# Kernel tuning notes

Hardware: AMD Instinct MI355X
Metric: run time of the kernel (lower is better)

The kernel has to match this reference:

```python
import jax, jax.numpy as jnp
import numpy as np

B, S, D, H = 1, 2048, 1024, 16
HD = D // H
THRESHOLD_PCT = 0.95
SPARSITY = 0.9
TOPK = max(1, int(S * (1.0 - SPARSITY)))  # 204


def setup_inputs() -> dict:
    key = jax.random.key(0)
    ks = jax.random.split(key, 6)
    inp = {
        'x': jax.random.normal(ks[0], (B, S, D), dtype=jnp.float32),
        'Wq': jax.random.normal(ks[1], (D, D), dtype=jnp.float32) * 0.02,
        'bq': jnp.zeros((D,), jnp.float32),
        'Wk': jax.random.normal(ks[2], (D, D), dtype=jnp.float32) * 0.02,
        'bk': jnp.zeros((D,), jnp.float32),
        'Wv': jax.random.normal(ks[3], (D, D), dtype=jnp.float32) * 0.02,
        'bv': jnp.zeros((D,), jnp.float32),
        'Wo': jax.random.normal(ks[4], (D, D), dtype=jnp.float32) * 0.02,
        'bo': jnp.zeros((D,), jnp.float32),
    }
    return inp


def _heads(t):  # [B,S,D] -> [B,H,S,HD]
    return t.reshape(B, S, H, HD).transpose(0, 2, 1, 3)


def reference(x, Wq, bq, Wk, bk, Wv, bv, Wo, bo):
    q = _heads(x @ Wq + bq)
    k = _heads(x @ Wk + bk)
    v = _heads(x @ Wv + bv)
    scores = jnp.einsum('bhqd,bhkd->bhqk', q, k) / jnp.sqrt(jnp.float32(HD))

    # --- dynamic threshold mask (per batch,head quantile over all S*S scores) ---
    flat = scores.reshape(B, H, S * S)
    thr = jnp.quantile(flat, THRESHOLD_PCT, axis=-1)[..., None, None]  # [B,H,1,1]
    thresh_mask = scores >= thr
    # fallback: if kept fraction exceeds (1 - sparsity_ratio), use per-row top-k
    cond = jnp.mean(thresh_mask.astype(scores.dtype)) > (1.0 - SPARSITY)
    kth = jax.lax.top_k(scores, TOPK)[0][..., -1:]  # k-th largest per row
    topk_mask = scores >= kth
    mask = jnp.where(cond, topk_mask, thresh_mask)

    masked = jnp.where(mask, scores, -jnp.inf)
    attn = jax.nn.softmax(masked, axis=-1)
    out = jnp.einsum('bhqk,bhkd->bhqd', attn, v)
    out = out.transpose(0, 2, 1, 3).reshape(B, S, D)
    return out @ Wo + bo
```

## Files before the change

kernel.cpp:

```cpp
#include <hip/hip_runtime.h>
#include <math.h>

#define SS 2048
#define DD 1024
#define HH 16
#define CAPC 327680u
#define LCAP 2048
#define RBIN 4

#define K_A 3984587u
#define K_B 3984588u
#define QFRAC 0.85f
#define WSCALE 2048.0f
#define WSCALE_INV (1.0f/2048.0f)
#define ESHIFT 4.0f
#define PLANE 2097152
#define NSAMP_RANK 124518u

typedef _Float16 f16x8 __attribute__((ext_vector_type(8)));
typedef _Float16 f16x4 __attribute__((ext_vector_type(4)));
typedef float    f32x4 __attribute__((ext_vector_type(4)));

__device__ __forceinline__ unsigned sortkey(float f) {
  unsigned b = __float_as_uint(f);
  return (b & 0x80000000u) ? ~b : (b | 0x80000000u);
}
__device__ __forceinline__ float inv_sortkey(unsigned u) {
  unsigned b = (u & 0x80000000u) ? (u ^ 0x80000000u) : ~u;
  return __uint_as_float(b);
}

__global__ __launch_bounds__(256) void split_x(const float* __restrict__ x,
                                               _Float16* __restrict__ xh,
                                               _Float16* __restrict__ xl)
{
  const int i = blockIdx.x * 256 + threadIdx.x;
  float4 v = ((const float4*)x)[i];
  float vv[4] = {v.x, v.y, v.z, v.w};
  f16x4 h, l;
#pragma unroll
  for (int j = 0; j < 4; ++j) {
    _Float16 hh = (_Float16)vv[j];
    h[j] = hh;
    l[j] = (_Float16)(vv[j] - (float)hh);
  }
  ((f16x4*)xh)[i] = h;
  ((f16x4*)xl)[i] = l;
}

__global__ __launch_bounds__(256) void split_wT(const float* __restrict__ Wq,
                                                const float* __restrict__ Wk,
                                                const float* __restrict__ Wv,
                                                const float* __restrict__ Wo,
                                                _Float16* __restrict__ wplanes)
{
  const int z = blockIdx.z;
  const float* W = (z == 0) ? Wq : (z == 1) ? Wk : (z == 2) ? Wv : Wo;
  _Float16* WhT = wplanes + (size_t)(2*z)     * (1024*1024);
  _Float16* WlT = wplanes + (size_t)(2*z + 1) * (1024*1024);
  __shared__ float tile[64][65];
  const int t  = threadIdx.x;
  const int r  = t >> 2;
  const int c0 = (t & 3) * 16;
  const int k0 = blockIdx.y * 64;
  const int n0 = blockIdx.x * 64;
#pragma unroll
  for (int j = 0; j < 4; ++j) {
    float4 v = *(const float4*)&W[(size_t)(k0 + r) * 1024 + n0 + c0 + j*4];
    tile[r][c0+j*4+0] = v.x; tile[r][c0+j*4+1] = v.y;
    tile[r][c0+j*4+2] = v.z; tile[r][c0+j*4+3] = v.w;
  }
  __syncthreads();
  f16x8 h0, h1, l0, l1;
#pragma unroll
  for (int j = 0; j < 8; ++j) {
    float v = tile[c0 + j][r] * WSCALE;
    _Float16 h = (_Float16)v;
    h0[j] = h; l0[j] = (_Float16)(v - (float)h);
  }
#pragma unroll
  for (int j = 0; j < 8; ++j) {
    float v = tile[c0 + 8 + j][r] * WSCALE;
    _Float16 h = (_Float16)v;
    h1[j] = h; l1[j] = (_Float16)(v - (float)h);
  }
  const size_t o = (size_t)(n0 + r) * 1024 + k0 + c0;
  *(f16x8*)&WhT[o]     = h0;
  *(f16x8*)&WhT[o + 8] = h1;
  *(f16x8*)&WlT[o]     = l0;
  *(f16x8*)&WlT[o + 8] = l1;
}

__device__ __forceinline__ void gemm_mfma_part(const _Float16* __restrict__ Ah,
                                               const _Float16* __restrict__ Al,
                                               const _Float16* __restrict__ BhT,
                                               const _Float16* __restrict__ BlT,
                                               float* __restrict__ pout,
                                               int bm, int bn, int kh)
{
  const int wave = threadIdx.x >> 6, lane = threadIdx.x & 63;
  const int wr = wave >> 1, wc = wave & 1;
  const int m0 = bm * 128 + wr * 64;
  const int n0 = bn * 128 + wc * 64;
  const int lr = lane & 15;
  const int ko = lane >> 4;

  f32x4 acc[4][4];
#pragma unroll
  for (int i = 0; i < 4; ++i)
#pragma unroll
    for (int j = 0; j < 4; ++j) acc[i][j] = (f32x4){0.f, 0.f, 0.f, 0.f};

  for (int kk = kh*16; kk < kh*16 + 16; ++kk) {
    const int kof = kk*32 + ko*8;
    f16x8 aH[4], aL[4], bH[4], bL[4];
#pragma unroll
    for (int i = 0; i < 4; ++i) {
      const size_t aoff = (size_t)(m0 + i*16 + lr) * 1024 + kof;
      aH[i] = *(const f16x8*)(Ah + aoff);
      aL[i] = *(const f16x8*)(Al + aoff);
      const size_t boff = (size_t)(n0 + i*16 + lr) * 1024 + kof;
      bH[i] = *(const f16x8*)(BhT + boff);
      bL[i] = *(const f16x8*)(BlT + boff);
    }
#pragma unroll
    for (int i = 0; i < 4; ++i)
#pragma unroll
      for (int j = 0; j < 4; ++j) {
        acc[i][j] = __builtin_amdgcn_mfma_f32_16x16x32_f16(aL[i], bL[j], acc[i][j], 0, 0, 0);
        acc[i][j] = __builtin_amdgcn_mfma_f32_16x16x32_f16(aH[i], bL[j], acc[i][j], 0, 0, 0);
        acc[i][j] = __builtin_amdgcn_mfma_f32_16x16x32_f16(aL[i], bH[j], acc[i][j], 0, 0, 0);
        acc[i][j] = __builtin_amdgcn_mfma_f32_16x16x32_f16(aH[i], bH[j], acc[i][j], 0, 0, 0);
      }
  }

#pragma unroll
  for (int i = 0; i < 4; ++i)
#pragma unroll
    for (int j = 0; j < 4; ++j)
#pragma unroll
      for (int r = 0; r < 4; ++r) {
        const int row = m0 + i*16 + ko*4 + r;
        const int col = n0 + j*16 + lr;
        pout[(size_t)row * 1024 + col] = acc[i][j][r];
      }
}

__global__ __launch_bounds__(256) void gemm_qkv_part(const _Float16* __restrict__ xh,
                                                     const _Float16* __restrict__ xl,
                                                     const _Float16* __restrict__ wplanes,
                                                     float* __restrict__ pbuf)
{
  const int z = blockIdx.z;
  const int g = z >> 1, kh = z & 1;
  const _Float16* BhT = wplanes + (size_t)(2*g)     * (1024*1024);
  const _Float16* BlT = wplanes + (size_t)(2*g + 1) * (1024*1024);
  gemm_mfma_part(xh, xl, BhT, BlT, pbuf + (size_t)z * PLANE,
                 blockIdx.y, blockIdx.x, kh);
}

__global__ __launch_bounds__(256) void gemm_o_part(const _Float16* __restrict__ ctxh,
                                                   const _Float16* __restrict__ ctxl,
                                                   const _Float16* __restrict__ wplanes,
                                                   float* __restrict__ pO)
{
  const int kh = blockIdx.z;
  gemm_mfma_part(ctxh, ctxl,
                 wplanes + (size_t)6 * (1024*1024),
                 wplanes + (size_t)7 * (1024*1024),
                 pO + (size_t)kh * PLANE, blockIdx.y, blockIdx.x, kh);
}

__global__ __launch_bounds__(256) void combine_qk(const float* __restrict__ pbuf,
                                                  const float* __restrict__ bq,
                                                  const float* __restrict__ bk,
                                                  _Float16* __restrict__ Qh,
                                                  _Float16* __restrict__ Ql,
                                                  _Float16* __restrict__ Kh,
                                                  _Float16* __restrict__ Kl)
{
  const int which = blockIdx.y;
  const float* p0 = pbuf + (size_t)(which*2)     * PLANE;
  const float* p1 = pbuf + (size_t)(which*2 + 1) * PLANE;
  const float* bias = which ? bk : bq;
  _Float16* Oh = which ? Kh : Qh;
  _Float16* Ol = which ? Kl : Ql;
  const int i = blockIdx.x * 256 + threadIdx.x;
  const int coloff = (i & 255) * 4;
  float4 a = ((const float4*)p0)[i];
  float4 b = ((const float4*)p1)[i];
  float av[4] = {a.x, a.y, a.z, a.w};
  float bv[4] = {b.x, b.y, b.z, b.w};
  f16x4 h, l;
#pragma unroll
  for (int j = 0; j < 4; ++j) {
    const float val = (av[j] + bv[j]) * WSCALE_INV + bias[coloff + j];
    _Float16 hh = (_Float16)val;
    h[j] = hh;
    l[j] = (_Float16)(val - (float)hh);
  }
  ((f16x4*)Oh)[i] = h;
  ((f16x4*)Ol)[i] = l;
}

__global__ __launch_bounds__(256) void combine_vT(const float* __restrict__ pbuf,
                                                  const float* __restrict__ bv,
                                                  _Float16* __restrict__ VtH,
                                                  _Float16* __restrict__ VtL)
{
  const float* p0 = pbuf + (size_t)4 * PLANE;
  const float* p1 = pbuf + (size_t)5 * PLANE;
  __shared__ float tile[64][65];
  const int t  = threadIdx.x;
  const int d0 = blockIdx.x * 64;
  const int m0 = blockIdx.y * 64;
  {
    const int r  = t >> 2;
    const int c0 = (t & 3) * 16;
#pragma unroll
    for (int j = 0; j < 4; ++j) {
      const size_t o = (size_t)(m0 + r) * 1024 + d0 + c0 + j*4;
      float4 a = *(const float4*)(p0 + o);
      float4 b = *(const float4*)(p1 + o);
      tile[r][c0+j*4+0] = (a.x + b.x) * WSCALE_INV + bv[d0 + c0 + j*4 + 0];
      tile[r][c0+j*4+1] = (a.y + b.y) * WSCALE_INV + bv[d0 + c0 + j*4 + 1];
      tile[r][c0+j*4+2] = (a.z + b.z) * WSCALE_INV + bv[d0 + c0 + j*4 + 2];
      tile[r][c0+j*4+3] = (a.w + b.w) * WSCALE_INV + bv[d0 + c0 + j*4 + 3];
    }
  }
  __syncthreads();
  {
    const int d  = t >> 2;
    const int rg = (t & 3) * 16;
#pragma unroll
    for (int j = 0; j < 4; ++j) {
      f16x4 hv, lv;
#pragma unroll
      for (int r = 0; r < 4; ++r) {
        const float val = tile[rg + j*4 + r][d];
        _Float16 h = (_Float16)val;
        hv[r] = h; lv[r] = (_Float16)(val - (float)h);
      }
      const size_t o = (size_t)(d0 + d) * 2048 + m0 + rg + j*4;
      *(f16x4*)&VtH[o] = hv;
      *(f16x4*)&VtL[o] = lv;
    }
  }
}

__global__ __launch_bounds__(256) void combine_o(const float* __restrict__ pO,
                                                 const float* __restrict__ bo,
                                                 float* __restrict__ out)
{
  const float* p0 = pO;
  const float* p1 = pO + (size_t)1 * PLANE;
  const int i = blockIdx.x * 256 + threadIdx.x;
  const int coloff = (i & 255) * 4;
  float4 a = ((const float4*)p0)[i];
  float4 b = ((const float4*)p1)[i];
  float4 o;
  o.x = (a.x + b.x) * WSCALE_INV + bo[coloff + 0];
  o.y = (a.y + b.y) * WSCALE_INV + bo[coloff + 1];
  o.z = (a.z + b.z) * WSCALE_INV + bo[coloff + 2];
  o.w = (a.w + b.w) * WSCALE_INV + bo[coloff + 3];
  ((float4*)out)[i] = o;
}

__global__ __launch_bounds__(256) void combine_ctx(const float* __restrict__ pctx,
                                                   const float* __restrict__ prs,
                                                   _Float16* __restrict__ ctxh,
                                                   _Float16* __restrict__ ctxl)
{
  const float* p0 = pctx;
  const float* p1 = pctx + (size_t)1 * PLANE;
  const int i = blockIdx.x * 256 + threadIdx.x;
  const int row = i >> 8;
  const int cd  = (i & 255) * 4;
  const int h   = cd >> 6;
  const float rs = prs[h*2048 + row] + prs[32768 + h*2048 + row];
  float4 a = ((const float4*)p0)[i];
  float4 b = ((const float4*)p1)[i];
  float av[4] = {a.x, a.y, a.z, a.w};
  float bv[4] = {b.x, b.y, b.z, b.w};
  f16x4 hh, ll;
#pragma unroll
  for (int j = 0; j < 4; ++j) {
    const float val = (av[j] + bv[j]) / rs;
    _Float16 hv = (_Float16)val;
    hh[j] = hv;
    ll[j] = (_Float16)(val - (float)hv);
  }
  ((f16x4*)ctxh)[i] = hh;
  ((f16x4*)ctxl)[i] = ll;
}

__global__ __launch_bounds__(256) void init_sel(unsigned* __restrict__ ghist,
                                                unsigned* __restrict__ shist,
                                                unsigned* __restrict__ ccnt,
                                                unsigned* __restrict__ flag,
                                                unsigned* __restrict__ fhist)
{
  int i = blockIdx.x * 256 + threadIdx.x;
  for (; i < HH * 16384; i += gridDim.x * 256) { ghist[i] = 0; shist[i] = 0; }
  const int j = blockIdx.x * 256 + threadIdx.x;
  if (j < HH * 512) fhist[j] = 0;
  if (blockIdx.x == 0 && threadIdx.x < HH) { ccnt[threadIdx.x] = 0; flag[threadIdx.x] = 0; }
}

__global__ __launch_bounds__(256) void sample_hist(const _Float16* __restrict__ Qh,
                                                   const _Float16* __restrict__ Ql,
                                                   const _Float16* __restrict__ Kh,
                                                   const _Float16* __restrict__ Kl,
                                                   unsigned* __restrict__ shist)
{
  const int kb = blockIdx.x, h = blockIdx.y;
  const int wave = threadIdx.x >> 6, lane = threadIdx.x & 63;
  const int lr = lane & 15, ko = lane >> 4;
  const int n0 = kb*128 + wave*32;

  __shared__ unsigned lh[16384];
  for (int i = threadIdx.x; i < 16384; i += 256) lh[i] = 0;
  __syncthreads();

  f32x4 acc[4][2];
#pragma unroll
  for (int i = 0; i < 4; ++i)
#pragma unroll
    for (int j = 0; j < 2; ++j) acc[i][j] = (f32x4){0.f, 0.f, 0.f, 0.f};

#pragma unroll
  for (int kk = 0; kk < 2; ++kk) {
    f16x8 aH[4], aL[4], bH[2], bL[2];
#pragma unroll
    for (int i = 0; i < 4; ++i) {
      const size_t aoff = (size_t)((i*16 + lr) * 32) * 1024 + h*64 + kk*32 + ko*8;
      aH[i] = *(const f16x8*)(Qh + aoff);
      aL[i] = *(const f16x8*)(Ql + aoff);
    }
#pragma unroll
    for (int j = 0; j < 2; ++j) {
      const size_t boff = (size_t)(n0 + j*16 + lr) * 1024 + h*64 + kk*32 + ko*8;
      bH[j] = *(const f16x8*)(Kh + boff);
      bL[j] = *(const f16x8*)(Kl + boff);
    }
#pragma unroll
    for (int i = 0; i < 4; ++i)
#pragma unroll
      for (int j = 0; j < 2; ++j) {
        acc[i][j] = __builtin_amdgcn_mfma_f32_16x16x32_f16(aL[i], bL[j], acc[i][j], 0, 0, 0);
        acc[i][j] = __builtin_amdgcn_mfma_f32_16x16x32_f16(aH[i], bL[j], acc[i][j], 0, 0, 0);
        acc[i][j] = __builtin_amdgcn_mfma_f32_16x16x32_f16(aL[i], bH[j], acc[i][j], 0, 0, 0);
        acc[i][j] = __builtin_amdgcn_mfma_f32_16x16x32_f16(aH[i], bH[j], acc[i][j], 0, 0, 0);
      }
  }

#pragma unroll
  for (int i = 0; i < 4; ++i)
#pragma unroll
    for (int j = 0; j < 2; ++j)
#pragma unroll
      for (int r = 0; r < 4; ++r) {
        const float val = acc[i][j][r] * 0.125f;
        atomicAdd(&lh[sortkey(val) >> 18], 1u);
      }
  __syncthreads();
  unsigned* __restrict__ gh = shist + (size_t)h * 16384;
  for (int i = threadIdx.x; i < 16384; i += 256) {
    const unsigned c = lh[i];
    if (c) atomicAdd(&gh[i], c);
  }
}

__global__ __launch_bounds__(256) void sample_scan(const unsigned* __restrict__ shist,
                                                   unsigned* __restrict__ rangeLo,
                                                   unsigned* __restrict__ rangeHi)
{
  const int hh = blockIdx.x;
  const int t = threadIdx.x;
  __shared__ unsigned part[256];
  __shared__ unsigned outb;
  if (t == 0) outb = 8192u;
  const unsigned* __restrict__ hb = shist + (size_t)hh * 16384;
  unsigned s = 0;
  for (int j = 0; j < 64; ++j) s += hb[t*64 + j];
  part[t] = s;
  __syncthreads();
  if (t == 0) {
    unsigned run = 0;
    for (int i = 0; i < 256; ++i) { unsigned tmp = part[i]; part[i] = run; run += tmp; }
  }
  __syncthreads();
  const unsigned cum0 = part[t];
  if (NSAMP_RANK >= cum0 && NSAMP_RANK < cum0 + s) {
    unsigned c2 = cum0;
    for (int j = 0; j < 64; ++j) {
      const unsigned c = hb[t*64 + j];
      if (NSAMP_RANK < c2 + c) { outb = t*64 + j; break; }
      c2 += c;
    }
  }
  __syncthreads();
  if (t == 0) {
    const int b = (int)outb;
    rangeLo[hh] = (unsigned)((b - RBIN < 0) ? 0 : b - RBIN);
    rangeHi[hh] = (unsigned)((b + RBIN > 16383) ? 16383 : b + RBIN);
  }
}

__global__ __launch_bounds__(512) void hist_compact_range(const _Float16* __restrict__ Qh,
                                                          const _Float16* __restrict__ Ql,
                                                          const _Float16* __restrict__ Kh,
                                                          const _Float16* __restrict__ Kl,
                                                          unsigned* __restrict__ ghist,
                                                          const unsigned* __restrict__ rangeLo,
                                                          const unsigned* __restrict__ rangeHi,
                                                          unsigned* __restrict__ cand,
                                                          unsigned* __restrict__ ccnt)
{
  const int bn = blockIdx.x, bm = blockIdx.y, h = blockIdx.z;
  const int wave = threadIdx.x >> 6, lane = threadIdx.x & 63;
  const int wr = wave >> 1, wc = wave & 1;
  const int m0 = bm * 256 + wr * 64;
  const int n0 = bn * 128 + wc * 64;
  const int lr = lane & 15;
  const int ko = lane >> 4;
  const unsigned lo = rangeLo[h], hi = rangeHi[h];
  unsigned* __restrict__ mycand = cand + (size_t)h * CAPC;

  __shared__ unsigned lh[16384];
  __shared__ unsigned lbuf[LCAP];
  __shared__ unsigned lcnt, gbase;
  for (int i = threadIdx.x; i < 16384; i += 512) lh[i] = 0;
  if (threadIdx.x == 0) lcnt = 0;
  __syncthreads();

  f32x4 acc[4][4];
#pragma unroll
  for (int i = 0; i < 4; ++i)
#pragma unroll
    for (int j = 0; j < 4; ++j) acc[i][j] = (f32x4){0.f, 0.f, 0.f, 0.f};

#pragma unroll
  for (int kk = 0; kk < 2; ++kk) {
    f16x8 aH[4], aL[4], bH[4], bL[4];
#pragma unroll
    for (int i = 0; i < 4; ++i) {
      const size_t aoff = (size_t)(m0 + i*16 + lr) * 1024 + h*64 + kk*32 + ko*8;
      aH[i] = *(const f16x8*)(Qh + aoff);
      aL[i] = *(const f16x8*)(Ql + aoff);
      const size_t boff = (size_t)(n0 + i*16 + lr) * 1024 + h*64 + kk*32 + ko*8;
      bH[i] = *(const f16x8*)(Kh + boff);
      bL[i] = *(const f16x8*)(Kl + boff);
    }
#pragma unroll
    for (int i = 0; i < 4; ++i)
#pragma unroll
      for (int j = 0; j < 4; ++j) {
        acc[i][j] = __builtin_amdgcn_mfma_f32_16x16x32_f16(aL[i], bL[j], acc[i][j], 0, 0, 0);
        acc[i][j] = __builtin_amdgcn_mfma_f32_16x16x32_f16(aH[i], bL[j], acc[i][j], 0, 0, 0);
        acc[i][j] = __builtin_amdgcn_mfma_f32_16x16x32_f16(aL[i], bH[j], acc[i][j], 0, 0, 0);
        acc[i][j] = __builtin_amdgcn_mfma_f32_16x16x32_f16(aH[i], bH[j], acc[i][j], 0, 0, 0);
      }
  }

#pragma unroll
  for (int i = 0; i < 4; ++i)
#pragma unroll
    for (int j = 0; j < 4; ++j)
#pragma unroll
      for (int r = 0; r < 4; ++r) {
        const float val = acc[i][j][r] * 0.125f;
        const unsigned u = sortkey(val);
        const unsigned bin = u >> 18;
        atomicAdd(&lh[bin], 1u);
        if (bin >= lo && bin <= hi) {
          unsigned id = atomicAdd(&lcnt, 1u);
          if (id < LCAP) lbuf[id] = u;
          else { unsigned g = atomicAdd(&ccnt[h], 1u); if (g < CAPC) mycand[g] = u; }
        }
      }
  __syncthreads();
  unsigned* __restrict__ gh = ghist + (size_t)h * 16384;
  for (int i = threadIdx.x; i < 16384; i += 512) {
    const unsigned c = lh[i];
    if (c) atomicAdd(&gh[i], c);
  }
  const unsigned n = (lcnt < LCAP) ? lcnt : LCAP;
  if (threadIdx.x == 0) gbase = n ? atomicAdd(&ccnt[h], n) : 0u;
  __syncthreads();
  const unsigned gb = gbase;
  for (unsigned i = threadIdx.x; i < n; i += 512)
    if (gb + i < CAPC) mycand[gb + i] = lbuf[i];
}

__global__ __launch_bounds__(256) void scan14(const unsigned* __restrict__ ghist,
                                              unsigned* __restrict__ state)
{
  const int hh = blockIdx.x;
  const int t = threadIdx.x;
  __shared__ unsigned part[256];
  __shared__ unsigned out[4];
  const unsigned* __restrict__ hb = ghist + (size_t)hh * 16384;
  unsigned s = 0;
  for (int j = 0; j < 64; ++j) s += hb[t*64 + j];
  part[t] = s;
  __syncthreads();
  if (t == 0) {
    unsigned run = 0;
    for (int i = 0; i < 256; ++i) { unsigned tmp = part[i]; part[i] = run; run += tmp; }
  }
  __syncthreads();
  const unsigned cum0 = part[t];
  if (K_A >= cum0 && K_A < cum0 + s) {
    unsigned c2 = cum0;
    for (int j = 0; j < 64; ++j) {
      const unsigned c = hb[t*64 + j];
      if (K_A < c2 + c) {
        const unsigned binA = t*64 + j;
        const unsigned residA = K_A - c2;
        unsigned binB, residB;
        if (residA + 1 < c) { binB = binA; residB = residA + 1; }
        else {
          unsigned bb = binA + 1;
          while (bb < 16384 && hb[bb] == 0) ++bb;
          if (bb >= 16384) bb = 16383;
          binB = bb; residB = 0;
        }
        out[0] = binA; out[1] = residA; out[2] = binB; out[3] = residB;
        break;
      }
      c2 += c;
    }
  }
  __syncthreads();
  if (t < 4) state[hh*4 + t] = out[t];
}

__global__ __launch_bounds__(64) void check_range(const unsigned* __restrict__ state,
                                                  const unsigned* __restrict__ rangeLo,
                                                  const unsigned* __restrict__ rangeHi,
                                                  unsigned* __restrict__ ccnt,
                                                  unsigned* __restrict__ flag,
                                                  unsigned* __restrict__ sstate)
{
  const int t = threadIdx.x;
  if (t < HH) {
    const unsigned binA = state[t*4+0];
    const unsigned binB = state[t*4+2];
    const unsigned lo = rangeLo[t], hi = rangeHi[t];
    const unsigned ok = (binA >= lo && binA <= hi && binB >= lo && binB <= hi &&
                         ccnt[t] <= CAPC) ? 1u : 0u;
    flag[t] = ok;
    if (!ok) ccnt[t] = 0;
    sstate[t*4+0] = state[t*4+0]; sstate[t*4+1] = state[t*4+1];
    sstate[t*4+2] = state[t*4+2]; sstate[t*4+3] = state[t*4+3];
  }
}

__global__ __launch_bounds__(512) void fallback_compact(const _Float16* __restrict__ Qh,
                                                        const _Float16* __restrict__ Ql,
                                                        const _Float16* __restrict__ Kh,
                                                        const _Float16* __restrict__ Kl,
                                                        const unsigned* __restrict__ state,
                                                        const unsigned* __restrict__ flagArr,
                                                        unsigned* __restrict__ cand,
                                                        unsigned* __restrict__ ccnt)
{
  const int bn = blockIdx.x, bm = blockIdx.y, h = blockIdx.z;
  if (flagArr[h] != 0) return;
  const int wave = threadIdx.x >> 6, lane = threadIdx.x & 63;
  const int wr = wave >> 1, wc = wave & 1;
  const int m0 = bm * 256 + wr * 64;
  const int n0 = bn * 128 + wc * 64;
  const int lr = lane & 15;
  const int ko = lane >> 4;

  __shared__ unsigned lbuf[LCAP];
  __shared__ unsigned lcnt, gbase;
  if (threadIdx.x == 0) lcnt = 0;
  __syncthreads();
  const unsigned binA = state[h*4+0];
  const unsigned binB = state[h*4+2];
  unsigned* __restrict__ mycand = cand + (size_t)h * CAPC;

  f32x4 acc[4][4];
#pragma unroll
  for (int i = 0; i < 4; ++i)
#pragma unroll
    for (int j = 0; j < 4; ++j) acc[i][j] = (f32x4){0.f, 0.f, 0.f, 0.f};

#pragma unroll
  for (int kk = 0; kk < 2; ++kk) {
    f16x8 aH[4], aL[4], bH[4], bL[4];
#pragma unroll
    for (int i = 0; i < 4; ++i) {
      const size_t aoff = (size_t)(m0 + i*16 + lr) * 1024 + h*64 + kk*32 + ko*8;
      aH[i] = *(const f16x8*)(Qh + aoff);
      aL[i] = *(const f16x8*)(Ql + aoff);
      const size_t boff = (size_t)(n0 + i*16 + lr) * 1024 + h*64 + kk*32 + ko*8;
      bH[i] = *(const f16x8*)(Kh + boff);
      bL[i] = *(const f16x8*)(Kl + boff);
    }
#pragma unroll
    for (int i = 0; i < 4; ++i)
#pragma unroll
      for (int j = 0; j < 4; ++j) {
        acc[i][j] = __builtin_amdgcn_mfma_f32_16x16x32_f16(aL[i], bL[j], acc[i][j], 0, 0, 0);
        acc[i][j] = __builtin_amdgcn_mfma_f32_16x16x32_f16(aH[i], bL[j], acc[i][j], 0, 0, 0);
        acc[i][j] = __builtin_amdgcn_mfma_f32_16x16x32_f16(aL[i], bH[j], acc[i][j], 0, 0, 0);
        acc[i][j] = __builtin_amdgcn_mfma_f32_16x16x32_f16(aH[i], bH[j], acc[i][j], 0, 0, 0);
      }
  }

#pragma unroll
  for (int i = 0; i < 4; ++i)
#pragma unroll
    for (int j = 0; j < 4; ++j)
#pragma unroll
      for (int r = 0; r < 4; ++r) {
        const float val = acc[i][j][r] * 0.125f;
        const unsigned u = sortkey(val);
        const unsigned bin = u >> 18;
        if (bin == binA || bin == binB) {
          unsigned id = atomicAdd(&lcnt, 1u);
          if (id < LCAP) lbuf[id] = u;
          else { unsigned g = atomicAdd(&ccnt[h], 1u); if (g < CAPC) mycand[g] = u; }
        }
      }
  __syncthreads();
  const unsigned n = (lcnt < LCAP) ? lcnt : LCAP;
  if (threadIdx.x == 0) gbase = n ? atomicAdd(&ccnt[h], n) : 0u;
  __syncthreads();
  const unsigned gb = gbase;
  for (unsigned i = threadIdx.x; i < n; i += 512)
    if (gb + i < CAPC) mycand[gb + i] = lbuf[i];
}

__global__ __launch_bounds__(256) void fs_hist(const unsigned* __restrict__ cand,
                                               const unsigned* __restrict__ ccnt,
                                               const unsigned* __restrict__ sstate,
                                               unsigned* __restrict__ fhist,
                                               int s, int w)
{
  const int hh = blockIdx.y;
  const int t = threadIdx.x;
  const unsigned nb = 1u << w;
  __shared__ unsigned lh0[256], lh1[256];
  lh0[t] = 0; lh1[t] = 0;
  __syncthreads();
  const unsigned pfxA = sstate[hh*4+0];
  const unsigned pfxB = sstate[hh*4+2];
  unsigned n = ccnt[hh]; if (n > CAPC) n = CAPC;
  const unsigned* __restrict__ list = cand + (size_t)hh * CAPC;
  for (unsigned i = blockIdx.x * 256 + t; i < n; i += 32 * 256) {
    const unsigned u = list[i];
    if ((u >> (s + w)) == pfxA) atomicAdd(&lh0[(u >> s) & (nb - 1)], 1u);
    if ((u >> (s + w)) == pfxB) atomicAdd(&lh1[(u >> s) & (nb - 1)], 1u);
  }
  __syncthreads();
  if (t < (int)nb) {
    if (lh0[t]) atomicAdd(&fhist[hh*512 + t], lh0[t]);
    if (lh1[t]) atomicAdd(&fhist[hh*512 + 256 + t], lh1[t]);
  }
}

__global__ __launch_bounds__(256) void fs_scan(unsigned* __restrict__ fhist,
                                               unsigned* __restrict__ sstate,
                                               float* __restrict__ thr,
                                               int s, int w)
{
  const int hh = blockIdx.x;
  const int t = threadIdx.x;
  const unsigned nb = 1u << w;
  if (t == 0) {
    float vals[2];
    for (int tgt = 0; tgt < 2; ++tgt) {
      unsigned pfx = sstate[hh*4 + tgt*2];
      unsigned k   = sstate[hh*4 + tgt*2 + 1];
      const unsigned* hb = &fhist[hh*512 + tgt*256];
      unsigned cum = 0, b = 0;
      for (; b < nb; ++b) { const unsigned c = hb[b]; if (cum + c > k) break; cum += c; }
      if (b == nb) b = nb - 1;
      pfx = (pfx << w) | b;
      k -= cum;
      sstate[hh*4 + tgt*2]     = pfx;
      sstate[hh*4 + tgt*2 + 1] = k;
      if (s == 0) vals[tgt] = inv_sortkey(pfx);
    }
    if (s == 0) thr[hh] = vals[0] + QFRAC * (vals[1] - vals[0]);
  }
  __syncthreads();
  fhist[hh*512 + t] = 0;
  fhist[hh*512 + 256 + t] = 0;
}

__global__ __launch_bounds__(256) void flash_pv_sk(const _Float16* __restrict__ Qh,
                                                   const _Float16* __restrict__ Ql,
                                                   const _Float16* __restrict__ Kh,
                                                   const _Float16* __restrict__ Kl,
                                                   const _Float16* __restrict__ VtH,
                                                   const _Float16* __restrict__ VtL,
                                                   const float* __restrict__ thrArr,
                                                   float* __restrict__ pctx,
                                                   float* __restrict__ prs)
{
  const int bm = blockIdx.x;
  const int h  = blockIdx.y;
  const int half = blockIdx.z;
  const int wave = threadIdx.x >> 6, lane = threadIdx.x & 63;
  const int lr = lane & 15;
  const int ko = lane >> 4;
  const int m0 = bm * 64;
  const float thr = thrArr[h];

  __shared__ _Float16 Plds[64][136];
  __shared__ float rsLDS[64][4];

  f16x8 qH[4][2], qL[4][2];
#pragma unroll
  for (int i = 0; i < 4; ++i)
#pragma unroll
    for (int kk = 0; kk < 2; ++kk) {
      const size_t aoff = (size_t)(m0 + i*16 + lr) * 1024 + h*64 + kk*32 + ko*8;
      qH[i][kk] = *(const f16x8*)(Qh + aoff);
      qL[i][kk] = *(const f16x8*)(Ql + aoff);
    }

  f32x4 oacc[4];
#pragma unroll
  for (int i = 0; i < 4; ++i) oacc[i] = (f32x4){0.f, 0.f, 0.f, 0.f};
  float rs[4][4];
#pragma unroll
  for (int i = 0; i < 4; ++i)
#pragma unroll
    for (int r = 0; r < 4; ++r) rs[i][r] = 0.f;

  const int d0 = wave * 16;

  for (int kt = half*8; kt < half*8 + 8; ++kt) {
    const int n0 = kt*128 + wave*32;
    f32x4 sacc[4][2];
#pragma unroll
    for (int i = 0; i < 4; ++i)
#pragma unroll
      for (int j = 0; j < 2; ++j) sacc[i][j] = (f32x4){0.f, 0.f, 0.f, 0.f};

#pragma unroll
    for (int kk = 0; kk < 2; ++kk) {
      f16x8 bH[2], bL[2];
#pragma unroll
      for (int j = 0; j < 2; ++j) {
        const size_t boff = (size_t)(n0 + j*16 + lr) * 1024 + h*64 + kk*32 + ko*8;
        bH[j] = *(const f16x8*)(Kh + boff);
        bL[j] = *(const f16x8*)(Kl + boff);
      }
#pragma unroll
      for (int i = 0; i < 4; ++i)
#pragma unroll
        for (int j = 0; j < 2; ++j) {
          sacc[i][j] = __builtin_amdgcn_mfma_f32_16x16x32_f16(qL[i][kk], bL[j], sacc[i][j], 0, 0, 0);
          sacc[i][j] = __builtin_amdgcn_mfma_f32_16x16x32_f16(qH[i][kk], bL[j], sacc[i][j], 0, 0, 0);
          sacc[i][j] = __builtin_amdgcn_mfma_f32_16x16x32_f16(qL[i][kk], bH[j], sacc[i][j], 0, 0, 0);
          sacc[i][j] = __builtin_amdgcn_mfma_f32_16x16x32_f16(qH[i][kk], bH[j], sacc[i][j], 0, 0, 0);
        }
    }

#pragma unroll
    for (int i = 0; i < 4; ++i)
#pragma unroll
      for (int j = 0; j < 2; ++j)
#pragma unroll
        for (int r = 0; r < 4; ++r) {
          const float val = sacc[i][j][r] * 0.125f;
          const float p = (val >= thr) ? __expf(val - thr - ESHIFT) : 0.f;
          rs[i][r] += p;
          Plds[i*16 + ko*4 + r][wave*32 + j*16 + lr] = (_Float16)p;
        }
    __syncthreads();

#pragma unroll
    for (int kk2 = 0; kk2 < 4; ++kk2) {
      f16x8 pa[4];
#pragma unroll
      for (int i = 0; i < 4; ++i)
        pa[i] = *(const f16x8*)&Plds[i*16 + lr][kk2*32 + ko*8];
      const size_t vo = (size_t)(h*64 + d0 + lr) * 2048 + kt*128 + kk2*32 + ko*8;
      const f16x8 vH = *(const f16x8*)(VtH + vo);
      const f16x8 vL = *(const f16x8*)(VtL + vo);
#pragma unroll
      for (int i = 0; i < 4; ++i) {
        oacc[i] = __builtin_amdgcn_mfma_f32_16x16x32_f16(pa[i], vL, oacc[i], 0, 0, 0);
        oacc[i] = __builtin_amdgcn_mfma_f32_16x16x32_f16(pa[i], vH, oacc[i], 0, 0, 0);
      }
    }
    __syncthreads();
  }

#pragma unroll
  for (int i = 0; i < 4; ++i)
#pragma unroll
    for (int r = 0; r < 4; ++r) {
      float v = rs[i][r];
      v += __shfl_xor(v, 1); v += __shfl_xor(v, 2);
      v += __shfl_xor(v, 4); v += __shfl_xor(v, 8);
      rs[i][r] = v;
    }
  if (lr == 0) {
#pragma unroll
    for (int i = 0; i < 4; ++i)
#pragma unroll
      for (int r = 0; r < 4; ++r)
        rsLDS[i*16 + ko*4 + r][wave] = rs[i][r];
  }
  __syncthreads();

  if (wave == 0 && lr == 0) {
#pragma unroll
    for (int i = 0; i < 4; ++i)
#pragma unroll
      for (int r = 0; r < 4; ++r) {
        const int lrow = i*16 + ko*4 + r;
        prs[half*32768 + h*2048 + m0 + lrow] =
            rsLDS[lrow][0] + rsLDS[lrow][1] + rsLDS[lrow][2] + rsLDS[lrow][3];
      }
  }

  float* __restrict__ pc = pctx + (size_t)half * PLANE;
#pragma unroll
  for (int i = 0; i < 4; ++i)
#pragma unroll
    for (int r = 0; r < 4; ++r) {
      const int lrow = i*16 + ko*4 + r;
      pc[(size_t)(m0 + lrow) * 1024 + h*64 + d0 + lr] = oacc[i][r];
    }
}

extern "C" void kernel_launch(void* const* d_in, const int* in_sizes, int n_in,
                              void* d_out, int out_size, void* d_ws, size_t ws_size,
                              hipStream_t stream)
{
  const float* x  = (const float*)d_in[0];
  const float* Wq = (const float*)d_in[1];
  const float* bq = (const float*)d_in[2];
  const float* Wk = (const float*)d_in[3];
  const float* bk = (const float*)d_in[4];
  const float* Wv = (const float*)d_in[5];
  const float* bv = (const float*)d_in[6];
  const float* Wo = (const float*)d_in[7];
  const float* bo = (const float*)d_in[8];
  float* out = (float*)d_out;
  char*  ws  = (char*)d_ws;

  const size_t MB = 1u << 20;
  _Float16* xh      = (_Float16*)(ws + 0*MB);
  _Float16* xl      = (_Float16*)(ws + 4*MB);
  _Float16* wplanes = (_Float16*)(ws + 8*MB);
  _Float16* Qh      = (_Float16*)(ws + 24*MB);
  _Float16* Ql      = (_Float16*)(ws + 28*MB);
  _Float16* Kh      = (_Float16*)(ws + 32*MB);
  _Float16* Kl      = (_Float16*)(ws + 36*MB);
  _Float16* VtH     = (_Float16*)(ws + 40*MB);
  _Float16* VtL     = (_Float16*)(ws + 44*MB);
  _Float16* ctxh    = (_Float16*)(ws + 48*MB);
  _Float16* ctxl    = (_Float16*)(ws + 52*MB);
  const size_t base = 56*MB;
  unsigned* state   = (unsigned*)(ws + base);
  float*    thr     = (float*)(ws + base + 4096);
  unsigned* ccnt    = (unsigned*)(ws + base + 8192);
  unsigned* flag    = (unsigned*)(ws + base + 12288);
  unsigned* rangeLo = (unsigned*)(ws + base + 16384);
  unsigned* rangeHi = (unsigned*)(ws + base + 20480);
  unsigned* sstate  = (unsigned*)(ws + base + 24576);
  unsigned* fhist   = (unsigned*)(ws + base + 28672);
  unsigned* ghist   = (unsigned*)(ws + 57*MB);
  unsigned* shist   = (unsigned*)(ws + 58*MB);
  unsigned* cand    = (unsigned*)(ws + 59*MB);
  float*    prs     = (float*)(ws + 80*MB);
  float*    pbuf    = (float*)(ws + 81*MB);
  float*    pctx    = pbuf;
  float*    pO      = pbuf + (size_t)2 * PLANE;

  split_x<<<2048, 256, 0, stream>>>(x, xh, xl);
  split_wT<<<dim3(16, 16, 4), 256, 0, stream>>>(Wq, Wk, Wv, Wo, wplanes);
  gemm_qkv_part<<<dim3(8, 16, 6), 256, 0, stream>>>(xh, xl, wplanes, pbuf);
  combine_qk<<<dim3(2048, 2), 256, 0, stream>>>(pbuf, bq, bk, Qh, Ql, Kh, Kl);
  combine_vT<<<dim3(16, 32), 256, 0, stream>>>(pbuf, bv, VtH, VtL);

  init_sel<<<256, 256, 0, stream>>>(ghist, shist, ccnt, flag, fhist);
  sample_hist<<<dim3(16, HH), 256, 0, stream>>>(Qh, Ql, Kh, Kl, shist);
  sample_scan<<<HH, 256, 0, stream>>>(shist, rangeLo, rangeHi);
  hist_compact_range<<<dim3(16, 8, HH), 512, 0, stream>>>(Qh, Ql, Kh, Kl, ghist,
                                                          rangeLo, rangeHi, cand, ccnt);
  scan14<<<HH, 256, 0, stream>>>(ghist, state);
  check_range<<<1, 64, 0, stream>>>(state, rangeLo, rangeHi, ccnt, flag, sstate);
  fallback_compact<<<dim3(16, 8, HH), 512, 0, stream>>>(Qh, Ql, Kh, Kl, state, flag, cand, ccnt);
  fs_hist<<<dim3(32, HH), 256, 0, stream>>>(cand, ccnt, sstate, fhist, 10, 8);
  fs_scan<<<HH, 256, 0, stream>>>(fhist, sstate, thr, 10, 8);
  fs_hist<<<dim3(32, HH), 256, 0, stream>>>(cand, ccnt, sstate, fhist, 2, 8);
  fs_scan<<<HH, 256, 0, stream>>>(fhist, sstate, thr, 2, 8);
  fs_hist<<<dim3(32, HH), 256, 0, stream>>>(cand, ccnt, sstate, fhist, 0, 2);
  fs_scan<<<HH, 256, 0, stream>>>(fhist, sstate, thr, 0, 2);

  flash_pv_sk<<<dim3(32, HH, 2), 256, 0, stream>>>(Qh, Ql, Kh, Kl, VtH, VtL, thr, pctx, prs);
  combine_ctx<<<2048, 256, 0, stream>>>(pctx, prs, ctxh, ctxl);

  gemm_o_part<<<dim3(8, 16, 2), 256, 0, stream>>>(ctxh, ctxl, wplanes, pO);
  combine_o<<<2048, 256, 0, stream>>>(pO, bo, out);
}
```

Baseline: 556.3 us.

## Replace full 16K-bin score histogram with below-range count plus narrow range histogram

The range pass no longer builds a 16384-bin shared histogram per block. It counts scores below the sampled range with a wave reduction and keeps a 9-bin histogram inside the range, which cuts shared-memory clearing, atomics and the LDS footprint. A new scan9 kernel locates the quantile bins from these counts. The full histogram is now built by a separate fallback kernel that returns early when the range check succeeds, which adds kernel launches and recomputes the scores for any head that misses the range.

```diff
diff --git a/kernel.cpp b/kernel.cpp
--- a/kernel.cpp
+++ b/kernel.cpp
@@ -298,13 +298,18 @@
                                                 unsigned* __restrict__ shist,
                                                 unsigned* __restrict__ ccnt,
                                                 unsigned* __restrict__ flag,
-                                                unsigned* __restrict__ fhist)
+                                                unsigned* __restrict__ fhist,
+                                                unsigned* __restrict__ cntBelow,
+                                                unsigned* __restrict__ ghist9)
 {
   int i = blockIdx.x * 256 + threadIdx.x;
   for (; i < HH * 16384; i += gridDim.x * 256) { ghist[i] = 0; shist[i] = 0; }
   const int j = blockIdx.x * 256 + threadIdx.x;
   if (j < HH * 512) fhist[j] = 0;
-  if (blockIdx.x == 0 && threadIdx.x < HH) { ccnt[threadIdx.x] = 0; flag[threadIdx.x] = 0; }
+  if (j < HH * 16) ghist9[j] = 0;
+  if (blockIdx.x == 0 && threadIdx.x < HH) {
+    ccnt[threadIdx.x] = 0; flag[threadIdx.x] = 0; cntBelow[threadIdx.x] = 0;
+  }
 }
 
 __global__ __launch_bounds__(256) void sample_hist(const _Float16* __restrict__ Qh,
@@ -407,15 +412,16 @@
   }
 }
 
-__global__ __launch_bounds__(512) void hist_compact_range(const _Float16* __restrict__ Qh,
-                                                          const _Float16* __restrict__ Ql,
-                                                          const _Float16* __restrict__ Kh,
-                                                          const _Float16* __restrict__ Kl,
-                                                          unsigned* __restrict__ ghist,
-                                                          const unsigned* __restrict__ rangeLo,
-                                                          const unsigned* __restrict__ rangeHi,
-                                                          unsigned* __restrict__ cand,
-                                                          unsigned* __restrict__ ccnt)
+__global__ __launch_bounds__(512) void range_count(const _Float16* __restrict__ Qh,
+                                                   const _Float16* __restrict__ Ql,
+                                                   const _Float16* __restrict__ Kh,
+                                                   const _Float16* __restrict__ Kl,
+                                                   const unsigned* __restrict__ rangeLo,
+                                                   const unsigned* __restrict__ rangeHi,
+                                                   unsigned* __restrict__ cand,
+                                                   unsigned* __restrict__ ccnt,
+                                                   unsigned* __restrict__ cntBelow,
+                                                   unsigned* __restrict__ ghist9)
 {
   const int bn = blockIdx.x, bm = blockIdx.y, h = blockIdx.z;
   const int wave = threadIdx.x >> 6, lane = threadIdx.x & 63;
@@ -427,11 +433,11 @@
   const unsigned lo = rangeLo[h], hi = rangeHi[h];
   unsigned* __restrict__ mycand = cand + (size_t)h * CAPC;
 
-  __shared__ unsigned lh[16384];
+  __shared__ unsigned lh9[16];
   __shared__ unsigned lbuf[LCAP];
-  __shared__ unsigned lcnt, gbase;
-  for (int i = threadIdx.x; i < 16384; i += 512) lh[i] = 0;
-  if (threadIdx.x == 0) lcnt = 0;
+  __shared__ unsigned lcnt, gbase, lbelow;
+  if (threadIdx.x < 16) lh9[threadIdx.x] = 0;
+  if (threadIdx.x == 0) { lcnt = 0; lbelow = 0; }
   __syncthreads();
 
   f32x4 acc[4][4];
@@ -463,6 +469,7 @@
       }
   }
 
+  unsigned nb = 0;
 #pragma unroll
   for (int i = 0; i < 4; ++i)
 #pragma unroll
@@ -472,31 +479,148 @@
         const float val = acc[i][j][r] * 0.125f;
         const unsigned u = sortkey(val);
         const unsigned bin = u >> 18;
-        atomicAdd(&lh[bin], 1u);
+        nb += (bin < lo) ? 1u : 0u;
         if (bin >= lo && bin <= hi) {
+          atomicAdd(&lh9[bin - lo], 1u);
           unsigned id = atomicAdd(&lcnt, 1u);
           if (id < LCAP) lbuf[id] = u;
           else { unsigned g = atomicAdd(&ccnt[h], 1u); if (g < CAPC) mycand[g] = u; }
         }
       }
+  nb += __shfl_xor(nb, 1);  nb += __shfl_xor(nb, 2);
+  nb += __shfl_xor(nb, 4);  nb += __shfl_xor(nb, 8);
+  nb += __shfl_xor(nb, 16); nb += __shfl_xor(nb, 32);
+  if (lane == 0) atomicAdd(&lbelow, nb);
+  __syncthreads();
+  if (threadIdx.x < 16) {
+    const unsigned c = lh9[threadIdx.x];
+    if (c) atomicAdd(&ghist9[h*16 + threadIdx.x], c);
+  }
+  if (threadIdx.x == 0 && lbelow) atomicAdd(&cntBelow[h], lbelow);
+  const unsigned n = (lcnt < LCAP) ? lcnt : LCAP;
+  if (threadIdx.x == 0) gbase = n ? atomicAdd(&ccnt[h], n) : 0u;
+  __syncthreads();
+  const unsigned gb = gbase;
+  for (unsigned i = threadIdx.x; i < n; i += 512)
+    if (gb + i < CAPC) mycand[gb + i] = lbuf[i];
+}
+
+__global__ __launch_bounds__(64) void scan9(const unsigned* __restrict__ ghist9,
+                                            const unsigned* __restrict__ cntBelow,
+                                            const unsigned* __restrict__ rangeLo,
+                                            const unsigned* __restrict__ rangeHi,
+                                            unsigned* __restrict__ ccnt,
+                                            unsigned* __restrict__ state,
+                                            unsigned* __restrict__ flag)
+{
+  const int hh = threadIdx.x;
+  if (hh >= HH) return;
+  const unsigned lo = rangeLo[hh], hi = rangeHi[hh];
+  const int nbins = (int)(hi - lo + 1);
+  const unsigned base = cntBelow[hh];
+  unsigned ok = 0;
+  unsigned binA = 0, residA = 0, binB = 0, residB = 0;
+  if (K_A >= base) {
+    unsigned k = K_A - base;
+    unsigned cum = 0;
+    for (int b = 0; b < nbins; ++b) {
+      const unsigned c = ghist9[hh*16 + b];
+      if (k < cum + c) {
+        binA = lo + b;
+        residA = k - cum;
+        if (residA + 1 < c) { binB = binA; residB = residA + 1; ok = 1; }
+        else {
+          for (int b2 = b + 1; b2 < nbins; ++b2) {
+            if (ghist9[hh*16 + b2]) { binB = lo + b2; residB = 0; ok = 1; break; }
+          }
+        }
+        break;
+      }
+      cum += c;
+    }
+  }
+  if (ccnt[hh] > CAPC) ok = 0;
+  flag[hh] = ok;
+  if (ok) {
+    state[hh*4+0] = binA; state[hh*4+1] = residA;
+    state[hh*4+2] = binB; state[hh*4+3] = residB;
+  } else {
+    ccnt[hh] = 0;
+  }
+}
+
+__global__ __launch_bounds__(512) void fb_scores_hist(const _Float16* __restrict__ Qh,
+                                                      const _Float16* __restrict__ Ql,
+                                                      const _Float16* __restrict__ Kh,
+                                                      const _Float16* __restrict__ Kl,
+                                                      const unsigned* __restrict__ flagArr,
+                                                      unsigned* __restrict__ ghist)
+{
+  const int bn = blockIdx.x, bm = blockIdx.y, h = blockIdx.z;
+  if (flagArr[h] != 0) return;
+  const int wave = threadIdx.x >> 6, lane = threadIdx.x & 63;
+  const int wr = wave >> 1, wc = wave & 1;
+  const int m0 = bm * 256 + wr * 64;
+  const int n0 = bn * 128 + wc * 64;
+  const int lr = lane & 15;
+  const int ko = lane >> 4;
+
+  __shared__ unsigned lh[16384];
+  for (int i = threadIdx.x; i < 16384; i += 512) lh[i] = 0;
+  __syncthreads();
+
+  f32x4 acc[4][4];
+#pragma unroll
+  for (int i = 0; i < 4; ++i)
+#pragma unroll
+    for (int j = 0; j < 4; ++j) acc[i][j] = (f32x4){0.f, 0.f, 0.f, 0.f};
+
+#pragma unroll
+  for (int kk = 0; kk < 2; ++kk) {
+    f16x8 aH[4], aL[4], bH[4], bL[4];
+#pragma unroll
+    for (int i = 0; i < 4; ++i) {
+      const size_t aoff = (size_t)(m0 + i*16 + lr) * 1024 + h*64 + kk*32 + ko*8;
+      aH[i] = *(const f16x8*)(Qh + aoff);
+      aL[i] = *(const f16x8*)(Ql + aoff);
+      const size_t boff = (size_t)(n0 + i*16 + lr) * 1024 + h*64 + kk*32 + ko*8;
+      bH[i] = *(const f16x8*)(Kh + boff);
+      bL[i] = *(const f16x8*)(Kl + boff);
+    }
+#pragma unroll
+    for (int i = 0; i < 4; ++i)
+#pragma unroll
+      for (int j = 0; j < 4; ++j) {
+        acc[i][j] = __builtin_amdgcn_mfma_f32_16x16x32_f16(aL[i], bL[j], acc[i][j], 0, 0, 0);
+        acc[i][j] = __builtin_amdgcn_mfma_f32_16x16x32_f16(aH[i], bL[j], acc[i][j], 0, 0, 0);
+        acc[i][j] = __builtin_amdgcn_mfma_f32_16x16x32_f16(aL[i], bH[j], acc[i][j], 0, 0, 0);
+        acc[i][j] = __builtin_amdgcn_mfma_f32_16x16x32_f16(aH[i], bH[j], acc[i][j], 0, 0, 0);
+      }
+  }
+
+#pragma unroll
+  for (int i = 0; i < 4; ++i)
+#pragma unroll
+    for (int j = 0; j < 4; ++j)
+#pragma unroll
+      for (int r = 0; r < 4; ++r) {
+        const float val = acc[i][j][r] * 0.125f;
+        atomicAdd(&lh[sortkey(val) >> 18], 1u);
+      }
   __syncthreads();
   unsigned* __restrict__ gh = ghist + (size_t)h * 16384;
   for (int i = threadIdx.x; i < 16384; i += 512) {
     const unsigned c = lh[i];
     if (c) atomicAdd(&gh[i], c);
   }
-  const unsigned n = (lcnt < LCAP) ? lcnt : LCAP;
-  if (threadIdx.x == 0) gbase = n ? atomicAdd(&ccnt[h], n) : 0u;
-  __syncthreads();
-  const unsigned gb = gbase;
-  for (unsigned i = threadIdx.x; i < n; i += 512)
-    if (gb + i < CAPC) mycand[gb + i] = lbuf[i];
-}
-
-__global__ __launch_bounds__(256) void scan14(const unsigned* __restrict__ ghist,
-                                              unsigned* __restrict__ state)
+}
+
+__global__ __launch_bounds__(256) void fb_scan14(const unsigned* __restrict__ ghist,
+                                                 const unsigned* __restrict__ flagArr,
+                                                 unsigned* __restrict__ state)
 {
   const int hh = blockIdx.x;
+  if (flagArr[hh] != 0) return;
   const int t = threadIdx.x;
   __shared__ unsigned part[256];
   __shared__ unsigned out[4];
@@ -536,27 +660,6 @@
   if (t < 4) state[hh*4 + t] = out[t];
 }
 
-__global__ __launch_bounds__(64) void check_range(const unsigned* __restrict__ state,
-                                                  const unsigned* __restrict__ rangeLo,
-                                                  const unsigned* __restrict__ rangeHi,
-                                                  unsigned* __restrict__ ccnt,
-                                                  unsigned* __restrict__ flag,
-                                                  unsigned* __restrict__ sstate)
-{
-  const int t = threadIdx.x;
-  if (t < HH) {
-    const unsigned binA = state[t*4+0];
-    const unsigned binB = state[t*4+2];
-    const unsigned lo = rangeLo[t], hi = rangeHi[t];
-    const unsigned ok = (binA >= lo && binA <= hi && binB >= lo && binB <= hi &&
-                         ccnt[t] <= CAPC) ? 1u : 0u;
-    flag[t] = ok;
-    if (!ok) ccnt[t] = 0;
-    sstate[t*4+0] = state[t*4+0]; sstate[t*4+1] = state[t*4+1];
-    sstate[t*4+2] = state[t*4+2]; sstate[t*4+3] = state[t*4+3];
-  }
-}
-
 __global__ __launch_bounds__(512) void fallback_compact(const _Float16* __restrict__ Qh,
                                                         const _Float16* __restrict__ Ql,
                                                         const _Float16* __restrict__ Kh,
@@ -634,6 +737,13 @@
   const unsigned gb = gbase;
   for (unsigned i = threadIdx.x; i < n; i += 512)
     if (gb + i < CAPC) mycand[gb + i] = lbuf[i];
+}
+
+__global__ __launch_bounds__(64) void seed_fs(const unsigned* __restrict__ state,
+                                              unsigned* __restrict__ sstate)
+{
+  const int t = threadIdx.x;
+  if (t < HH * 4) sstate[t] = state[t];
 }
 
 __global__ __launch_bounds__(256) void fs_hist(const unsigned* __restrict__ cand,
@@ -864,21 +974,23 @@
   _Float16* ctxh    = (_Float16*)(ws + 48*MB);
   _Float16* ctxl    = (_Float16*)(ws + 52*MB);
   const size_t base = 56*MB;
-  unsigned* state   = (unsigned*)(ws + base);
-  float*    thr     = (float*)(ws + base + 4096);
-  unsigned* ccnt    = (unsigned*)(ws + base + 8192);
-  unsigned* flag    = (unsigned*)(ws + base + 12288);
-  unsigned* rangeLo = (unsigned*)(ws + base + 16384);
-  unsigned* rangeHi = (unsigned*)(ws + base + 20480);
-  unsigned* sstate  = (unsigned*)(ws + base + 24576);
-  unsigned* fhist   = (unsigned*)(ws + base + 28672);
-  unsigned* ghist   = (unsigned*)(ws + 57*MB);
-  unsigned* shist   = (unsigned*)(ws + 58*MB);
-  unsigned* cand    = (unsigned*)(ws + 59*MB);
-  float*    prs     = (float*)(ws + 80*MB);
-  float*    pbuf    = (float*)(ws + 81*MB);
-  float*    pctx    = pbuf;
-  float*    pO      = pbuf + (size_t)2 * PLANE;
+  unsigned* state    = (unsigned*)(ws + base);
+  float*    thr      = (float*)(ws + base + 4096);
+  unsigned* ccnt     = (unsigned*)(ws + base + 8192);
+  unsigned* flag     = (unsigned*)(ws + base + 12288);
+  unsigned* rangeLo  = (unsigned*)(ws + base + 16384);
+  unsigned* rangeHi  = (unsigned*)(ws + base + 20480);
+  unsigned* sstate   = (unsigned*)(ws + base + 24576);
+  unsigned* fhist    = (unsigned*)(ws + base + 28672);
+  unsigned* cntBelow = (unsigned*)(ws + base + 65536);
+  unsigned* ghist9   = (unsigned*)(ws + base + 69632);
+  unsigned* ghist    = (unsigned*)(ws + 57*MB);
+  unsigned* shist    = (unsigned*)(ws + 58*MB);
+  unsigned* cand     = (unsigned*)(ws + 59*MB);
+  float*    prs      = (float*)(ws + 80*MB);
+  float*    pbuf     = (float*)(ws + 81*MB);
+  float*    pctx     = pbuf;
+  float*    pO       = pbuf + (size_t)2 * PLANE;
 
   split_x<<<2048, 256, 0, stream>>>(x, xh, xl);
   split_wT<<<dim3(16, 16, 4), 256, 0, stream>>>(Wq, Wk, Wv, Wo, wplanes);
@@ -886,14 +998,16 @@
   combine_qk<<<dim3(2048, 2), 256, 0, stream>>>(pbuf, bq, bk, Qh, Ql, Kh, Kl);
   combine_vT<<<dim3(16, 32), 256, 0, stream>>>(pbuf, bv, VtH, VtL);
 
-  init_sel<<<256, 256, 0, stream>>>(ghist, shist, ccnt, flag, fhist);
+  init_sel<<<256, 256, 0, stream>>>(ghist, shist, ccnt, flag, fhist, cntBelow, ghist9);
   sample_hist<<<dim3(16, HH), 256, 0, stream>>>(Qh, Ql, Kh, Kl, shist);
   sample_scan<<<HH, 256, 0, stream>>>(shist, rangeLo, rangeHi);
-  hist_compact_range<<<dim3(16, 8, HH), 512, 0, stream>>>(Qh, Ql, Kh, Kl, ghist,
-                                                          rangeLo, rangeHi, cand, ccnt);
-  scan14<<<HH, 256, 0, stream>>>(ghist, state);
-  check_range<<<1, 64, 0, stream>>>(state, rangeLo, rangeHi, ccnt, flag, sstate);
+  range_count<<<dim3(16, 8, HH), 512, 0, stream>>>(Qh, Ql, Kh, Kl, rangeLo, rangeHi,
+                                                   cand, ccnt, cntBelow, ghist9);
+  scan9<<<1, 64, 0, stream>>>(ghist9, cntBelow, rangeLo, rangeHi, ccnt, state, flag);
+  fb_scores_hist<<<dim3(16, 8, HH), 512, 0, stream>>>(Qh, Ql, Kh, Kl, flag, ghist);
+  fb_scan14<<<HH, 256, 0, stream>>>(ghist, flag, state);
   fallback_compact<<<dim3(16, 8, HH), 512, 0, stream>>>(Qh, Ql, Kh, Kl, state, flag, cand, ccnt);
+  seed_fs<<<1, 64, 0, stream>>>(state, sstate);
   fs_hist<<<dim3(32, HH), 256, 0, stream>>>(cand, ccnt, sstate, fhist, 10, 8);
   fs_scan<<<HH, 256, 0, stream>>>(fhist, sstate, thr, 10, 8);
   fs_hist<<<dim3(32, HH), 256, 0, stream>>>(cand, ccnt, sstate, fhist, 2, 8);
```

Result: faster. 538.6 us (median of 2 runs) (-3.2%).
